# Kernel optimization log

Measured on AMD Instinct MI355X. Metric: run time of the kernel, lower is better.

The kernel has to match this reference:

```python
import jax, jax.numpy as jnp
import numpy as np

BLANK = 0


def _rnnt_neg_log_like(acts, labels, act_lens, label_lens):
    """RNN-T loss (sum over batch), matching warp-transducer cpu_rnnt.

    acts: (B, T, U+1, V) raw logits (log-softmax applied internally).
    labels: (B, U) int targets (padded; padding never read for the loss).
    act_lens: (B,) valid T per example. label_lens: (B,) valid U per example.
    """
    lp = jax.nn.log_softmax(acts, axis=-1)            # (B, T, U1, V)
    blank_lp = lp[..., BLANK]                          # (B, T, U1)
    U = labels.shape[1]
    # emit log-prob of the u-th label at lattice node (t, u): (B, T, U)
    emit_lp = jnp.take_along_axis(lp[:, :, :U, :], labels[:, None, :, None], axis=3)[..., 0]

    def per_seq(blank_b, emit_b, T_b, U_b):
        # blank_b: (T, U1), emit_b: (T, U)
        zero = jnp.zeros((1,), emit_b.dtype)
        # row t=0: alpha[0, u] = sum_{j<u} emit[0, j]
        alpha0 = jnp.concatenate([zero, jnp.cumsum(emit_b[0])])  # (U1,)

        def step(alpha_prev, inputs):
            bl_prev, em_t = inputs
            # a[u] = alpha[t-1, u] + log P(blank | t-1, u)
            a = alpha_prev + bl_prev
            # prefix sums of emit probs along this row: C[u] = sum_{j<u} emit[t, j]
            C = jnp.concatenate([zero, jnp.cumsum(em_t)])
            # alpha[t, u] = logsumexp_{k<=u} (a[k] + C[u] - C[k])  (stable log-domain scan)
            alpha = C + jax.lax.cumlogsumexp(a - C)
            return alpha, alpha

        _, rest = jax.lax.scan(step, alpha0, (blank_b[:-1], emit_b[1:]))
        alphas = jnp.concatenate([alpha0[None], rest], axis=0)   # (T, U1)
        # Padded lattice region is never read: recursion is causal in (t, u).
        ll = alphas[T_b - 1, U_b] + blank_b[T_b - 1, U_b]
        return -ll

    costs = jax.vmap(per_seq)(blank_lp, emit_lp, act_lens, label_lens)  # (B,)
    return jnp.sum(costs)  # size_average=False -> sum of per-example costs


def setup_inputs() -> dict:
    key = jax.random.key(0)
    k1, k2, k3, k4 = jax.random.split(key, 4)
    B, T, U, V = 8, 200, 100, 512
    acts = jax.random.normal(k1, (B, T, U + 1, V), dtype=jnp.float32)
    labels = jax.random.randint(k2, (B, U), 1, V, dtype=jnp.int64)  # non-blank labels
    act_lens = jax.random.randint(k3, (B,), T // 2, T + 1, dtype=jnp.int32)
    label_lens = jax.random.randint(k4, (B,), U // 2, U + 1, dtype=jnp.int32)
    return {"acts": acts, "labels": labels, "act_lens": act_lens, "label_lens": label_lens}


def reference(acts, labels, act_lens, label_lens):
    return _rnnt_neg_log_like(acts, labels, act_lens, label_lens)
```

## Files before the change

kernel.cpp:

```cpp
#include <hip/hip_runtime.h>
#include <math.h>

#define BB 8
#define TT 200
#define UU 100
#define U1 101
#define VV 512
#define PS 102
#define NEG_BIG (-1.0e30f)
#define L2E 1.4426950408889634f
#define LN2 0.6931471805599453f

__device__ __forceinline__ float exp2_fast(float x) { return __builtin_amdgcn_exp2f(x); }

template<int CTRL, int RM>
__device__ __forceinline__ float dppf(float old, float x) {
    return __int_as_float(__builtin_amdgcn_update_dpp(
        __float_as_int(old), __float_as_int(x), CTRL, RM, 0xF, false));
}

__device__ __forceinline__ float lae2(float x, float y) {
    float d = x - y;
    float e = exp2_fast(-fabsf(d));
    return fmaxf(x, y) + __log2f(1.0f + e);
}

__device__ __forceinline__ float laescan(float x) {
    x = lae2(x, dppf<0x111, 0xF>(NEG_BIG, x));
    x = lae2(x, dppf<0x112, 0xF>(NEG_BIG, x));
    x = lae2(x, dppf<0x114, 0xF>(NEG_BIG, x));
    x = lae2(x, dppf<0x118, 0xF>(NEG_BIG, x));
    x = lae2(x, dppf<0x142, 0xA>(NEG_BIG, x));
    x = lae2(x, dppf<0x143, 0xC>(NEG_BIG, x));
    return x;
}
__device__ __forceinline__ float addscan(float x) {
    x = x + dppf<0x111, 0xF>(0.0f, x);
    x = x + dppf<0x112, 0xF>(0.0f, x);
    x = x + dppf<0x114, 0xF>(0.0f, x);
    x = x + dppf<0x118, 0xF>(0.0f, x);
    x = x + dppf<0x142, 0xA>(0.0f, x);
    x = x + dppf<0x143, 0xC>(0.0f, x);
    return x;
}

__device__ __forceinline__ float wave_shr1(float x, bool c1648, bool c32) {
    float t   = dppf<0x111, 0xF>(NEG_BIG, x);
    float b15 = dppf<0x142, 0xA>(NEG_BIG, x);
    float b31 = dppf<0x143, 0x4>(NEG_BIG, x);
    float e = c1648 ? b15 : t;
    return c32 ? b31 : e;
}

__global__ __launch_bounds__(256) void row_lse_kernel(
    const float* __restrict__ acts, const int* __restrict__ labels,
    const int* __restrict__ act_lens, const int* __restrict__ label_lens,
    float* __restrict__ blank_lp, float* __restrict__ emit_lp)
{
    const int wave = (blockIdx.x << 2) | ((int)threadIdx.x >> 6);
    const int lane = threadIdx.x & 63;
    if (wave >= BB * TT * U1) return;

    const int u  = wave % U1;
    const int bt = wave / U1;
    const int b  = bt / TT;
    const int t  = bt % TT;
    const int Ub = label_lens[b];
    if (t >= act_lens[b] || u > Ub) return;

    const float* row = acts + (size_t)wave * VV;
    float4 a = ((const float4*)row)[lane];
    float4 c = ((const float4*)row)[lane + 64];

    float m = fmaxf(fmaxf(fmaxf(a.x, a.y), fmaxf(a.z, a.w)),
                    fmaxf(fmaxf(c.x, c.y), fmaxf(c.z, c.w)));
    #pragma unroll
    for (int off = 32; off; off >>= 1)
        m = fmaxf(m, __shfl_xor(m, off, 64));

    float s = __expf(a.x - m) + __expf(a.y - m) + __expf(a.z - m) + __expf(a.w - m)
            + __expf(c.x - m) + __expf(c.y - m) + __expf(c.z - m) + __expf(c.w - m);
    #pragma unroll
    for (int off = 32; off; off >>= 1)
        s += __shfl_xor(s, off, 64);

    const float denom = m + __logf(s);

    float x0 = __shfl(a.x, 0, 64);
    if (lane == 0) blank_lp[bt * PS + u] = (x0 - denom) * L2E;

    if (u < UU) {
        int lbl = labels[b * UU + u];
        int e   = lbl & 3;
        int src = (lbl >> 2) & 63;
        float4 s4 = (lbl < 256) ? a : c;
        float cand = (e == 0) ? s4.x : (e == 1) ? s4.y : (e == 2) ? s4.z : s4.w;
        float xl = __shfl(cand, src, 64);
        if (lane == 0) emit_lp[bt * PS + u] = (xl - denom) * L2E;
    }
}

__global__ __launch_bounds__(64) void alpha_kernel(
    const float* __restrict__ blank_lp, const float* __restrict__ emit_lp,
    const int* __restrict__ act_lens, const int* __restrict__ label_lens,
    float* __restrict__ out)
{
    const int b    = blockIdx.x;
    const int lane = threadIdx.x;
    const float* bl = blank_lp + b * TT * PS;
    const float* em = emit_lp  + b * TT * PS;
    const int Tb = act_lens[b];
    const int Ub = label_lens[b];

    const int  ll    = (lane < 50) ? lane : 50;
    const bool c1648 = (lane == 16) || (lane == 48);
    const bool c32   = (lane == 32);

    const float blfin = bl[(Tb - 1) * PS + Ub];

    auto load2 = [&](const float* base) -> float2 {
        return ((const float2*)base)[ll];
    };

    float a0, a1;
    {
        float2 e = load2(em);
        float q = e.x + e.y;
        float S = addscan(q);
        a1 = S - e.y; a0 = S - q;
    }
    float Cc0, Cc1;
    {
        float2 e = load2(em + PS);
        float q = e.x + e.y;
        float S = addscan(q);
        Cc1 = S - e.y; Cc0 = S - q;
    }
    float2 em_nx  = load2(em + 2 * PS);
    float2 bl_cur = load2(bl);

    for (int t = 1; t < Tb; ++t) {
        float2 bl_nx = load2(bl + t * PS);
        float2 em_n2 = (t + 2 < TT) ? load2(em + (t + 2) * PS)
                                    : make_float2(0.f, 0.f);

        float qn  = em_nx.x + em_nx.y;
        float Sn  = addscan(qn);
        float Cn1 = Sn - em_nx.y, Cn0 = Sn - qn;

        float z0 = a0 + bl_cur.x - Cc0;
        float z1 = a1 + bl_cur.y - Cc1;
        float p  = lae2(z0, z1);
        float S  = laescan(p);
        float E  = wave_shr1(S, c1648, c32);
        float s0 = lae2(E, z0);
        float s1 = lae2(s0, z1);
        a0 = Cc0 + s0;
        a1 = Cc1 + s1;

        bl_cur = bl_nx; em_nx = em_n2; Cc0 = Cn0; Cc1 = Cn1;
    }

    float rsel = (Ub & 1) ? a1 : a0;
    float res  = __shfl(rsel, Ub >> 1, 64);
    if (lane == 0)
        atomicAdd(out, -(res + blfin) * LN2);
}

extern "C" void kernel_launch(void* const* d_in, const int* in_sizes, int n_in,
                              void* d_out, int out_size, void* d_ws, size_t ws_size,
                              hipStream_t stream) {
    const float* acts       = (const float*)d_in[0];
    const int*   labels     = (const int*)d_in[1];
    const int*   act_lens   = (const int*)d_in[2];
    const int*   label_lens = (const int*)d_in[3];
    float* out = (float*)d_out;

    float* blank_lp = (float*)d_ws;
    float* emit_lp  = blank_lp + BB * TT * PS;

    const int nrows   = BB * TT * U1;
    const int blocks1 = (nrows + 3) / 4;

    (void)hipMemsetAsync(d_out, 0, (size_t)out_size * sizeof(float), stream);
    row_lse_kernel<<<blocks1, 256, 0, stream>>>(acts, labels, act_lens, label_lens,
                                                blank_lp, emit_lp);
    alpha_kernel<<<BB, 64, 0, stream>>>(blank_lp, emit_lp, act_lens, label_lens, out);
}
```

Baseline: 497.1 us.

## Switch alpha recursion to anti-diagonal wavefront with skewed layout and prefetch ring

```diff
diff --git a/kernel.cpp b/kernel.cpp
--- a/kernel.cpp
+++ b/kernel.cpp
@@ -7,6 +7,8 @@
 #define U1 101
 #define VV 512
 #define PS 102
+#define ND 320
+#define PF 8
 #define NEG_BIG (-1.0e30f)
 #define L2E 1.4426950408889634f
 #define LN2 0.6931471805599453f
@@ -23,25 +25,6 @@
     float d = x - y;
     float e = exp2_fast(-fabsf(d));
     return fmaxf(x, y) + __log2f(1.0f + e);
-}
-
-__device__ __forceinline__ float laescan(float x) {
-    x = lae2(x, dppf<0x111, 0xF>(NEG_BIG, x));
-    x = lae2(x, dppf<0x112, 0xF>(NEG_BIG, x));
-    x = lae2(x, dppf<0x114, 0xF>(NEG_BIG, x));
-    x = lae2(x, dppf<0x118, 0xF>(NEG_BIG, x));
-    x = lae2(x, dppf<0x142, 0xA>(NEG_BIG, x));
-    x = lae2(x, dppf<0x143, 0xC>(NEG_BIG, x));
-    return x;
-}
-__device__ __forceinline__ float addscan(float x) {
-    x = x + dppf<0x111, 0xF>(0.0f, x);
-    x = x + dppf<0x112, 0xF>(0.0f, x);
-    x = x + dppf<0x114, 0xF>(0.0f, x);
-    x = x + dppf<0x118, 0xF>(0.0f, x);
-    x = x + dppf<0x142, 0xA>(0.0f, x);
-    x = x + dppf<0x143, 0xC>(0.0f, x);
-    return x;
 }
 
 __device__ __forceinline__ float wave_shr1(float x, bool c1648, bool c32) {
@@ -86,8 +69,10 @@
 
     const float denom = m + __logf(s);
 
+    const int dn = (b * ND + t + u) * PS + u;
+
     float x0 = __shfl(a.x, 0, 64);
-    if (lane == 0) blank_lp[bt * PS + u] = (x0 - denom) * L2E;
+    if (lane == 0) blank_lp[dn] = (x0 - denom) * L2E;
 
     if (u < UU) {
         int lbl = labels[b * UU + u];
@@ -96,7 +81,7 @@
         float4 s4 = (lbl < 256) ? a : c;
         float cand = (e == 0) ? s4.x : (e == 1) ? s4.y : (e == 2) ? s4.z : s4.w;
         float xl = __shfl(cand, src, 64);
-        if (lane == 0) emit_lp[bt * PS + u] = (xl - denom) * L2E;
+        if (lane == 0) emit_lp[dn] = (xl - denom) * L2E;
     }
 }
 
@@ -107,62 +92,52 @@
 {
     const int b    = blockIdx.x;
     const int lane = threadIdx.x;
-    const float* bl = blank_lp + b * TT * PS;
-    const float* em = emit_lp  + b * TT * PS;
+    const float* bl = blank_lp + (size_t)b * ND * PS;
+    const float* em = emit_lp  + (size_t)b * ND * PS;
     const int Tb = act_lens[b];
     const int Ub = label_lens[b];
+    const int nfin = Tb - 1 + Ub;
 
     const int  ll    = (lane < 50) ? lane : 50;
     const bool c1648 = (lane == 16) || (lane == 48);
     const bool c32   = (lane == 32);
 
-    const float blfin = bl[(Tb - 1) * PS + Ub];
+    const float blfin = bl[nfin * PS + Ub];
 
-    auto load2 = [&](const float* base) -> float2 {
-        return ((const float2*)base)[ll];
+    auto load2 = [&](const float* base, int row) -> float2 {
+        return ((const float2*)(base + row * PS))[ll];
     };
 
-    float a0, a1;
-    {
-        float2 e = load2(em);
-        float q = e.x + e.y;
-        float S = addscan(q);
-        a1 = S - e.y; a0 = S - q;
-    }
-    float Cc0, Cc1;
-    {
-        float2 e = load2(em + PS);
-        float q = e.x + e.y;
-        float S = addscan(q);
-        Cc1 = S - e.y; Cc0 = S - q;
-    }
-    float2 em_nx  = load2(em + 2 * PS);
-    float2 bl_cur = load2(bl);
-
-    for (int t = 1; t < Tb; ++t) {
-        float2 bl_nx = load2(bl + t * PS);
-        float2 em_n2 = (t + 2 < TT) ? load2(em + (t + 2) * PS)
-                                    : make_float2(0.f, 0.f);
-
-        float qn  = em_nx.x + em_nx.y;
-        float Sn  = addscan(qn);
-        float Cn1 = Sn - em_nx.y, Cn0 = Sn - qn;
-
-        float z0 = a0 + bl_cur.x - Cc0;
-        float z1 = a1 + bl_cur.y - Cc1;
-        float p  = lae2(z0, z1);
-        float S  = laescan(p);
-        float E  = wave_shr1(S, c1648, c32);
-        float s0 = lae2(E, z0);
-        float s1 = lae2(s0, z1);
-        a0 = Cc0 + s0;
-        a1 = Cc1 + s1;
-
-        bl_cur = bl_nx; em_nx = em_n2; Cc0 = Cn0; Cc1 = Cn1;
+    float2 blb[PF], emb[PF];
+    #pragma unroll
+    for (int k = 0; k < PF; ++k) {
+        blb[k] = load2(bl, k);
+        emb[k] = load2(em, k);
     }
 
-    float rsel = (Ub & 1) ? a1 : a0;
-    float res  = __shfl(rsel, Ub >> 1, 64);
+    float a0 = (lane == 0) ? 0.0f : NEG_BIG;
+    float a1 = NEG_BIG;
+    float rcap = NEG_BIG;
+
+    for (int n0 = 1; n0 <= nfin; n0 += PF) {
+        #pragma unroll
+        for (int k = 0; k < PF; ++k) {
+            const int n = n0 + k;
+            float b0  = a0 + blb[k].x;
+            float b1  = a1 + blb[k].y;
+            float ein = a0 + emb[k].x;
+            float y   = a1 + emb[k].y;
+            float esh = wave_shr1(y, c1648, c32);
+            a0 = lae2(b0, esh);
+            a1 = lae2(b1, ein);
+            if (n == nfin) rcap = (Ub & 1) ? a1 : a0;
+            const int nr = n - 1 + PF;
+            blb[k] = load2(bl, nr);
+            emb[k] = load2(em, nr);
+        }
+    }
+
+    float res = __shfl(rcap, Ub >> 1, 64);
     if (lane == 0)
         atomicAdd(out, -(res + blfin) * LN2);
 }
@@ -177,7 +152,7 @@
     float* out = (float*)d_out;
 
     float* blank_lp = (float*)d_ws;
-    float* emit_lp  = blank_lp + BB * TT * PS;
+    float* emit_lp  = blank_lp + BB * ND * PS;
 
     const int nrows   = BB * TT * U1;
     const int blocks1 = (nrows + 3) / 4;
```

New measurement: 437.4 us. 1.14x faster.
